# Kernel optimization log

Measured on AMD Instinct MI355X. Metric: run time of the kernel, lower is better.

Reference implementation:

```python
import jax, jax.numpy as jnp
import numpy as np

EMBED_DIM = 512
NUM_HEADS = 8
B, L_Q, L_K = 2, 2048, 2048


def setup_inputs() -> dict:
    key = jax.random.key(0)
    ks = jax.random.split(key, 8)
    s = 0.02  # weight init scale
    return {
        "query": jax.random.normal(ks[0], (B, L_Q, EMBED_DIM), jnp.float32),
        "key":   jax.random.normal(ks[1], (B, L_K, EMBED_DIM), jnp.float32),
        "value": jax.random.normal(ks[2], (B, L_K, EMBED_DIM), jnp.float32),
        "wq": jax.random.normal(ks[3], (EMBED_DIM, EMBED_DIM), jnp.float32) * s,
        "wk": jax.random.normal(ks[4], (EMBED_DIM, EMBED_DIM), jnp.float32) * s,
        "wv": jax.random.normal(ks[5], (EMBED_DIM, EMBED_DIM), jnp.float32) * s,
        "bq": jnp.zeros((EMBED_DIM,), jnp.float32),
        "bk": jnp.zeros((EMBED_DIM,), jnp.float32),
        "bv": jnp.zeros((EMBED_DIM,), jnp.float32),
        "wo": jax.random.normal(ks[6], (EMBED_DIM, EMBED_DIM), jnp.float32) * s,
        "bo": jnp.zeros((EMBED_DIM,), jnp.float32),
    }


def _prob_sparse_mask(query, key, num_heads):
    # Faithful to _prob_QK: max-mean sparsity score, top-k query selection,
    # gather of reduced queries, reduced QK matmul (vectorized, no python loops).
    Bq, Lq, D = query.shape
    Lk = key.shape[1]
    dh = D // num_heads
    n_top = int(np.log(Lk))  # int(np.ceil/np.log) as in source forward: int(np.log(L_K))
    Q = query.reshape(Bq, Lq, num_heads, dh)
    K = key.reshape(Bq, Lk, num_heads, dh)
    Qh = jnp.transpose(Q, (0, 2, 1, 3))                      # [B,H,Lq,dh]
    # NOTE: source does K.transpose(1,2).reshape(B,H,D,L_K) -- a reshape, not a
    # transpose of the last two dims. We replicate that exactly.
    Kr = jnp.transpose(K, (0, 2, 1, 3)).reshape(Bq, num_heads, dh, Lk)  # [B,H,dh,Lk]
    QK = jnp.einsum('bhqd,bhdk->bhqk', Qh, Kr)               # [B,H,Lq,Lk]
    M = QK.max(-1) - QK.sum(-1) / Lk                         # max-mean score [B,H,Lq]
    _, M_top = jax.lax.top_k(M, n_top)                       # [B,H,n_top]
    Q_red = jnp.take_along_axis(Qh, M_top[..., None], axis=2)  # [B,H,n_top,dh]
    QK_red = jnp.einsum('bhtd,bhdk->bhtk', Q_red, Kr)        # [B,H,n_top,Lk]
    # Scatter reduced rows back into a full additive attn mask (zeros elsewhere).
    mask = jnp.zeros((Bq, num_heads, Lq, Lk), QK.dtype)
    bi = jnp.arange(Bq)[:, None, None]
    hi = jnp.arange(num_heads)[None, :, None]
    return mask.at[bi, hi, M_top].set(QK_red)


def reference(query, key, value, wq, wk, wv, bq, bk, bv, wo, bo):
    Bq, Lq, D = query.shape
    Lk = key.shape[1]
    H = NUM_HEADS
    dh = D // H
    mask = _prob_sparse_mask(query, key, H)                  # [B,H,Lq,Lk]
    q = (query @ wq.T + bq).reshape(Bq, Lq, H, dh).transpose(0, 2, 1, 3)
    k = (key @ wk.T + bk).reshape(Bq, Lk, H, dh).transpose(0, 2, 1, 3)
    v = (value @ wv.T + bv).reshape(Bq, Lk, H, dh).transpose(0, 2, 1, 3)
    scores = jnp.einsum('bhqd,bhkd->bhqk', q, k) * (dh ** -0.5) + mask
    attn = jax.nn.softmax(scores, axis=-1)                   # dropout inactive (eval)
    out = jnp.einsum('bhqk,bhkd->bhqd', attn, v)
    out = out.transpose(0, 2, 1, 3).reshape(Bq, Lq, D)
    return out @ wo.T + bo
```

## Files before the change

kernel.cpp:

```cpp
#include <hip/hip_runtime.h>

#define DEV static __device__ __forceinline__

typedef short s16;
typedef __attribute__((ext_vector_type(4))) short short4_t;
typedef __attribute__((ext_vector_type(8))) short short8;
typedef __attribute__((ext_vector_type(4))) float f32x4;

#define NB 2
#define NH 8
#define SL 2048
#define DM 512
#define DH 64
#define NTOP 7
#define LOG2E 1.4426950408889634f
#define NROWS (NB*NH*SL)
#define FSPLIT 2
#define SSPLIT 2

DEV short f2bf(float x){
  union { float f; unsigned u; } v; v.f = x;
  unsigned r = v.u + 0x7fffu + ((v.u >> 16) & 1u);
  return (short)(r >> 16);
}
DEV float bf2f(short b){
  union { float f; unsigned u; } v; v.u = ((unsigned)(unsigned short)b) << 16;
  return v.f;
}
DEV f32x4 mfma16(short8 a, short8 b, f32x4 c){
  return __builtin_amdgcn_mfma_f32_16x16x32_bf16(a, b, c, 0, 0, 0);
}
DEV unsigned cvtpk(float lo, float hi){
  unsigned r;
  asm("v_cvt_pk_bf16_f32 %0, %1, %2" : "=v"(r) : "v"(lo), "v"(hi));
  return r;
}
DEV void gl2lds16(const s16* g, s16* l){
  __builtin_amdgcn_global_load_lds(
      (const __attribute__((address_space(1))) unsigned*)g,
      (__attribute__((address_space(3))) unsigned*)l, 16, 0, 0);
}

__global__ void prep_kernel(const float* __restrict__ query, const float* __restrict__ key,
    const float* __restrict__ value,
    const float* __restrict__ wq, const float* __restrict__ wk,
    const float* __restrict__ wv, const float* __restrict__ wo,
    s16* __restrict__ q_hi, s16* __restrict__ q_lo, s16* __restrict__ xk, s16* __restrict__ xv,
    s16* __restrict__ khi, s16* __restrict__ klo,
    s16* __restrict__ wqb, s16* __restrict__ wkb, s16* __restrict__ wvb, s16* __restrict__ wob){
  const int nbb = (NB*SL*DM)/256;
  const int wbb = (DM*DM)/256;
  __shared__ s16 thi[64][66];
  __shared__ s16 tlo[64][66];
  int bid = blockIdx.x;
  int t = threadIdx.x;
  if (bid < nbb){
    int i = bid*256 + t;
    float v = query[i];
    short h = f2bf(v);
    q_hi[i] = h;
    q_lo[i] = f2bf(v - bf2f(h));
    return;
  }
  bid -= nbb;
  if (bid < nbb){ int i = bid*256 + t; xk[i] = f2bf(key[i]); return; }
  bid -= nbb;
  if (bid < nbb){ int i = bid*256 + t; xv[i] = f2bf(value[i]); return; }
  bid -= nbb;
  if (bid < 512){
    int k6 = bid & 31, h = (bid >> 5) & 7, b = bid >> 8;
    int kl = t & 63, dq = t >> 6;
    #pragma unroll
    for (int dd = 0; dd < 16; ++dd){
      int d = dd*4 + dq;
      float v = key[((size_t)b*SL + d*32 + k6)*DM + h*DH + kl];
      short hh = f2bf(v);
      thi[d][kl] = hh;
      tlo[d][kl] = f2bf(v - bf2f(hh));
    }
    __syncthreads();
    int d2 = t & 63, kq = t >> 6;
    size_t obase = (((size_t)(b*NH + h))*SL + (size_t)k6*64)*DH;
    #pragma unroll
    for (int kk = 0; kk < 16; ++kk){
      int kl2 = kk*4 + kq;
      khi[obase + (size_t)kl2*DH + d2] = thi[d2][kl2];
      klo[obase + (size_t)kl2*DH + d2] = tlo[d2][kl2];
    }
    return;
  }
  bid -= 512;
  if (bid < wbb){ int i = bid*256 + t; wqb[i] = f2bf(wq[i]); return; }
  bid -= wbb;
  if (bid < wbb){ int i = bid*256 + t; wkb[i] = f2bf(wk[i]); return; }
  bid -= wbb;
  if (bid < wbb){ int i = bid*256 + t; wvb[i] = f2bf(wv[i]); return; }
  bid -= wbb;
  if (bid < wbb){ int i = bid*256 + t; wob[i] = f2bf(wo[i]); return; }
}

__global__ __launch_bounds__(256) void vpt_kernel(const s16* __restrict__ Vp, s16* __restrict__ VpT){
  __shared__ s16 tl[64][66];
  int bid = blockIdx.x;
  int k6 = bid & 31, h = (bid >> 5) & 7, b = bid >> 8;
  int t = threadIdx.x;
  int d = t & 63, kq = t >> 6;
  #pragma unroll
  for (int kk = 0; kk < 16; ++kk){
    int kl = kk*4 + kq;
    tl[kl][d] = Vp[((size_t)b*SL + k6*64 + kl)*DM + h*DH + d];
  }
  __syncthreads();
  int kl2 = t & 63, dq = t >> 6;
  size_t obase = ((size_t)(b*NH + h))*DH*SL + (size_t)k6*64;
  #pragma unroll
  for (int dd = 0; dd < 16; ++dd){
    int d2 = dd*4 + dq;
    VpT[obase + (size_t)d2*SL + kl2] = tl[kl2][d2];
  }
}

template<int OUTF32>
DEV void gemm_body(const s16* __restrict__ A, const s16* __restrict__ Bw,
        const float* __restrict__ bias, void* __restrict__ Cout, int bid, int tid, float scale){
  __shared__ __align__(16) s16 Abuf[2][128*64];
  __shared__ __align__(16) s16 Bbuf[2][64*64];
  int nt = bid >> 3, ot = bid & 7;
  int w = tid >> 6, l = tid & 63;
  int lr = l & 15, lg = l >> 4;
  int n0 = nt*128, o0 = ot*64;
  auto stage = [&](int cur, int kg){
    #pragma unroll
    for (int i = 0; i < 4; ++i){
      int r = w*32 + i*8 + (l>>3);
      int cs = (l&7) ^ (r&7);
      gl2lds16(A + (size_t)(n0 + r)*DM + kg + cs*8, &Abuf[cur][(w*32 + i*8)*64]);
    }
    #pragma unroll
    for (int i = 0; i < 2; ++i){
      int r = w*16 + i*8 + (l>>3);
      int cs = (l&7) ^ (r&7);
      gl2lds16(Bw + (size_t)(o0 + r)*DM + kg + cs*8, &Bbuf[cur][(w*16 + i*8)*64]);
    }
  };
  f32x4 acc[2][4] = {};
  stage(0, 0);
  __syncthreads();
  const int NIT = DM/64;
  for (int it = 0; it < NIT; ++it){
    int cur = it & 1;
    if (it + 1 < NIT) stage(cur^1, (it+1)*64);
    #pragma unroll
    for (int kc = 0; kc < 2; ++kc){
      short8 a0 = *(const short8*)&Abuf[cur][(w*32 +      lr)*64 + ((kc*4+lg) ^ (lr&7))*8];
      short8 a1 = *(const short8*)&Abuf[cur][(w*32 + 16 + lr)*64 + ((kc*4+lg) ^ (lr&7))*8];
      #pragma unroll
      for (int c = 0; c < 4; ++c){
        short8 bf = *(const short8*)&Bbuf[cur][(c*16 + lr)*64 + ((kc*4+lg) ^ (lr&7))*8];
        acc[0][c] = mfma16(a0, bf, acc[0][c]);
        acc[1][c] = mfma16(a1, bf, acc[1][c]);
      }
    }
    __syncthreads();
  }
  #pragma unroll
  for (int sub = 0; sub < 2; ++sub)
    #pragma unroll
    for (int c = 0; c < 4; ++c){
      int col = o0 + c*16 + lr;
      float bb = bias[col];
      #pragma unroll
      for (int j = 0; j < 4; ++j){
        int row = n0 + w*32 + sub*16 + lg*4 + j;
        float v = (acc[sub][c][j] + bb)*scale;
        if (OUTF32) ((float*)Cout)[(size_t)row*DM + col] = v;
        else        ((s16*) Cout)[(size_t)row*DM + col] = f2bf(v);
      }
    }
}

__global__ __launch_bounds__(256) void gemm_proj(const s16* __restrict__ Aq, const s16* __restrict__ Ak,
        const s16* __restrict__ Av, const s16* __restrict__ Wq, const s16* __restrict__ Wk,
        const s16* __restrict__ Wv, const float* __restrict__ bq, const float* __restrict__ bk,
        const float* __restrict__ bv, s16* __restrict__ Oq, s16* __restrict__ Ok, s16* __restrict__ Ov){
  int which = blockIdx.x >> 8;
  const s16* A  = which == 0 ? Aq : which == 1 ? Ak : Av;
  const s16* Bw = which == 0 ? Wq : which == 1 ? Wk : Wv;
  const float* bias = which == 0 ? bq : which == 1 ? bk : bv;
  s16* C = which == 0 ? Oq : which == 1 ? Ok : Ov;
  float scale = which == 0 ? 0.125f*LOG2E : 1.0f;
  gemm_body<0>(A, Bw, bias, C, blockIdx.x & 255, threadIdx.x, scale);
}

__global__ __launch_bounds__(256) void gemm_out(const s16* __restrict__ A, const s16* __restrict__ Bw,
        const float* __restrict__ bias, float* __restrict__ Cout){
  gemm_body<1>(A, Bw, bias, Cout, blockIdx.x, threadIdx.x, 1.0f);
}

__global__ __launch_bounds__(256) void stats_kernel(const s16* __restrict__ qhi, const s16* __restrict__ qlo,
        const s16* __restrict__ khi, const s16* __restrict__ klo,
        float* __restrict__ Mmx, float* __restrict__ Msm){
  __shared__ __align__(16) s16 Hbuf[2][64*64];
  __shared__ __align__(16) s16 Lbuf[2][64*64];
  int bid = blockIdx.x;
  int s = bid & 1, qt = (bid >> 1) & 31, h = (bid >> 6) & 7, b = bid >> 9;
  int tid = threadIdx.x;
  int w = tid >> 6, l = tid & 63;
  int lr = l & 15, lg = l >> 4;
  int dx = lr & 7;
  int q0 = qt*64 + w*16;
  const s16* qp  = qhi + ((size_t)b*SL + q0 + lr)*DM + h*DH + lg*8;
  const s16* qlp = qlo + ((size_t)b*SL + q0 + lr)*DM + h*DH + lg*8;
  short8 qh0 = *(const short8*)qp;
  short8 qh1 = *(const short8*)(qp + 32);
  short8 ql0 = *(const short8*)qlp;
  short8 ql1 = *(const short8*)(qlp + 32);
  const s16* kb  = khi + ((size_t)b*NH + h)*SL*DH;
  const s16* klb = klo + ((size_t)b*NH + h)*SL*DH;
  auto stage = [&](int cur, int kg){
    #pragma unroll
    for (int i = 0; i < 2; ++i){
      int r = w*16 + i*8 + (l>>3);
      int cs = (l&7) ^ (r&7);
      gl2lds16(kb  + (size_t)(kg + r)*DH + cs*8, &Hbuf[cur][(w*16 + i*8)*64]);
    }
    #pragma unroll
    for (int i = 0; i < 2; ++i){
      int r = w*16 + i*8 + (l>>3);
      int cs = (l&7) ^ (r&7);
      gl2lds16(klb + (size_t)(kg + r)*DH + cs*8, &Lbuf[cur][(w*16 + i*8)*64]);
    }
  };
  float mx = -1e30f, sm = 0.f;
  int kbeg = s*(SL/SSPLIT);
  const int NIT = (SL/SSPLIT)/64;
  stage(0, kbeg);
  __syncthreads();
  for (int it = 0; it < NIT; ++it){
    int cur = it & 1;
    if (it + 1 < NIT) stage(cur^1, kbeg + (it+1)*64);
    #pragma unroll
    for (int t = 0; t < 4; ++t){
      int rb = (t*16 + lr)*64;
      short8 kh0 = *(const short8*)&Hbuf[cur][rb + ((  lg) ^ dx)*8];
      short8 kh1 = *(const short8*)&Hbuf[cur][rb + ((4+lg) ^ dx)*8];
      short8 kl0 = *(const short8*)&Lbuf[cur][rb + ((  lg) ^ dx)*8];
      short8 kl1 = *(const short8*)&Lbuf[cur][rb + ((4+lg) ^ dx)*8];
      f32x4 sacc = {};
      sacc = mfma16(kh0, qh0, sacc);
      sacc = mfma16(kh1, qh1, sacc);
      sacc = mfma16(kl0, qh0, sacc);
      sacc = mfma16(kl1, qh1, sacc);
      sacc = mfma16(kh0, ql0, sacc);
      sacc = mfma16(kh1, ql1, sacc);
      #pragma unroll
      for (int j = 0; j < 4; ++j){ mx = fmaxf(mx, sacc[j]); sm += sacc[j]; }
    }
    __syncthreads();
  }
  mx = fmaxf(mx, __shfl_xor(mx, 16));
  mx = fmaxf(mx, __shfl_xor(mx, 32));
  sm += __shfl_xor(sm, 16);
  sm += __shfl_xor(sm, 32);
  if (lg == 0){
    size_t row = ((size_t)b*NH + h)*SL + q0 + lr;
    Mmx[(size_t)s*NROWS + row] = mx;
    Msm[(size_t)s*NROWS + row] = sm;
  }
}

__global__ __launch_bounds__(64) void topk_kernel(const float* __restrict__ Mmx,
        const float* __restrict__ Msm, int* __restrict__ topidx, int* __restrict__ rowsel){
  int bh = blockIdx.x;
  int l = threadIdx.x;
  __shared__ float smv[SL];
  size_t base = (size_t)bh*SL;
  for (int i = l; i < SL; i += 64){
    float mx = Mmx[base + i];
    float sm = Msm[base + i];
    #pragma unroll
    for (int s = 1; s < SSPLIT; ++s){
      mx = fmaxf(mx, Mmx[(size_t)s*NROWS + base + i]);
      sm += Msm[(size_t)s*NROWS + base + i];
    }
    smv[i] = mx - sm*(1.0f/SL);
    rowsel[base + i] = -1;
  }
  __syncthreads();
  for (int t = 0; t < NTOP; ++t){
    float bvv = -1e38f; int bi = SL;
    for (int i = l; i < SL; i += 64){
      float v = smv[i];
      if (v > bvv){ bvv = v; bi = i; }
    }
    for (int off = 32; off >= 1; off >>= 1){
      float ov = __shfl_xor(bvv, off);
      int oi = __shfl_xor(bi, off);
      if (ov > bvv || (ov == bvv && oi < bi)){ bvv = ov; bi = oi; }
    }
    if (l == 0){
      topidx[bh*8 + t] = bi;
      rowsel[base + bi] = t;
    }
    smv[bi] = -1e38f;
    __syncthreads();
  }
}

__global__ __launch_bounds__(256) void maskrow_kernel(const float* __restrict__ query,
        const float* __restrict__ key, const int* __restrict__ topidx, float* __restrict__ maskrows){
  __shared__ float tile[64][65];
  __shared__ float qs[NTOP][64];
  int bid = blockIdx.x;
  int k6 = bid & 31, h = (bid >> 5) & 7, b = bid >> 8;
  int bh = b*NH + h;
  int t = threadIdx.x;
  int kl = t & 63, w = t >> 6;
  for (int i = t; i < NTOP*64; i += 256){
    int tt = i >> 6, d = i & 63;
    qs[tt][d] = query[((size_t)b*SL + topidx[bh*8 + tt])*DM + h*DH + d];
  }
  #pragma unroll
  for (int dd = 0; dd < 16; ++dd){
    int d = dd*4 + w;
    tile[d][kl] = key[((size_t)b*SL + d*32 + k6)*DM + h*DH + kl];
  }
  __syncthreads();
  for (int tt = w; tt < NTOP; tt += 4){
    float acc = 0.f;
    #pragma unroll
    for (int d = 0; d < 64; ++d)
      acc = fmaf(qs[tt][d], tile[d][kl], acc);
    maskrows[((size_t)bh*NTOP + tt)*SL + k6*64 + kl] = acc*LOG2E;
  }
}

__global__ __launch_bounds__(256) void flash_kernel(const s16* __restrict__ Qp, const s16* __restrict__ Kp,
        const s16* __restrict__ VpT, const float* __restrict__ maskrows, const int* __restrict__ rowsel,
        float* __restrict__ Opart, float* __restrict__ lpart){
  __shared__ __align__(16) s16 Kbuf[2][64*64];
  __shared__ __align__(16) s16 Vbuf[2][64*64];
  int bid = blockIdx.x;
  int s = bid & 1, qt = (bid >> 1) & 31, h = (bid >> 6) & 7, b = bid >> 9;
  int tid = threadIdx.x;
  int w = tid >> 6, l = tid & 63;
  int lr = l & 15, lg = l >> 4;
  int dx = lr & 7;
  int q0 = qt*64 + w*16;
  int bh = b*NH + h;
  const s16* qp = Qp + ((size_t)b*SL + q0 + lr)*DM + h*DH + lg*8;
  short8 bq0 = *(const short8*)qp;
  short8 bq1 = *(const short8*)(qp + 32);
  int sel = rowsel[(size_t)bh*SL + q0 + lr];
  const float* mrow = maskrows + ((size_t)bh*NTOP + (sel >= 0 ? sel : 0))*SL;
  const s16* kpb = Kp + (size_t)b*SL*DM + h*DH;
  const s16* vtb = VpT + (size_t)bh*DH*SL;
  auto stage = [&](int cur, int kg){
    #pragma unroll
    for (int i = 0; i < 2; ++i){
      int r = w*16 + i*8 + (l>>3);
      int cs = (l&7) ^ (r&7);
      gl2lds16(kpb + (size_t)(kg + r)*DM + cs*8, &Kbuf[cur][(w*16 + i*8)*64]);
    }
    #pragma unroll
    for (int i = 0; i < 2; ++i){
      int d = w*16 + i*8 + (l>>3);
      int cs = (l&7) ^ (d&7);
      gl2lds16(vtb + (size_t)d*SL + kg + cs*8, &Vbuf[cur][(w*16 + i*8)*64]);
    }
  };
  f32x4 acc[4] = {};
  float lsum = 0.f;
  int kbeg = s*(SL/FSPLIT);
  const int NIT = (SL/FSPLIT)/64;
  stage(0, kbeg);
  __syncthreads();
  for (int it = 0; it < NIT; ++it){
    int cur = it & 1;
    if (it + 1 < NIT) stage(cur^1, kbeg + (it+1)*64);
    int k0 = kbeg + it*64;
    float pv[4][4];
    #pragma unroll
    for (int t = 0; t < 4; ++t){
      int rb = (t*16 + lr)*64;
      short8 ka0 = *(const short8*)&Kbuf[cur][rb + ((  lg) ^ dx)*8];
      short8 ka1 = *(const short8*)&Kbuf[cur][rb + ((4+lg) ^ dx)*8];
      f32x4 sc = {};
      sc = mfma16(ka0, bq0, sc);
      sc = mfma16(ka1, bq1, sc);
      #pragma unroll
      for (int j = 0; j < 4; ++j) pv[t][j] = sc[j];
    }
    if (sel >= 0){
      #pragma unroll
      for (int t = 0; t < 4; ++t)
        #pragma unroll
        for (int j = 0; j < 4; ++j)
          pv[t][j] += mrow[k0 + t*16 + lg*4 + j];
    }
    #pragma unroll
    for (int t = 0; t < 4; ++t)
      #pragma unroll
      for (int j = 0; j < 4; ++j){
        float pp = exp2f(pv[t][j]);
        pv[t][j] = pp;
        lsum += pp;
      }
    short8 paf[2];
    #pragma unroll
    for (int kt = 0; kt < 2; ++kt){
      union { unsigned u[4]; short8 s8; } uu;
      uu.u[0] = cvtpk(pv[2*kt][0],   pv[2*kt][1]);
      uu.u[1] = cvtpk(pv[2*kt][2],   pv[2*kt][3]);
      uu.u[2] = cvtpk(pv[2*kt+1][0], pv[2*kt+1][1]);
      uu.u[3] = cvtpk(pv[2*kt+1][2], pv[2*kt+1][3]);
      paf[kt] = uu.s8;
    }
    #pragma unroll
    for (int c = 0; c < 4; ++c){
      const s16* vb = &Vbuf[cur][(c*16 + lr)*64];
      #pragma unroll
      for (int kt = 0; kt < 2; ++kt){
        short4_t lo = *(const short4_t*)&vb[((8*kt   + lg) ^ (dx<<1))*4];
        short4_t hi = *(const short4_t*)&vb[((8*kt+4 + lg) ^ (dx<<1))*4];
        short8 vf = __builtin_shufflevector(lo, hi, 0, 1, 2, 3, 4, 5, 6, 7);
        acc[c] = mfma16(vf, paf[kt], acc[c]);
      }
    }
    __syncthreads();
  }
  lsum += __shfl_xor(lsum, 16);
  lsum += __shfl_xor(lsum, 32);
  size_t row = (size_t)bh*SL + q0 + lr;
  float* Op = Opart + ((size_t)s*NROWS + row)*DH;
  #pragma unroll
  for (int c = 0; c < 4; ++c)
    *(f32x4*)(Op + c*16 + lg*4) = acc[c];
  if (lg == 0)
    lpart[(size_t)s*NROWS + row] = lsum;
}

__global__ __launch_bounds__(256) void flash_combine(const float* __restrict__ Opart,
        const float* __restrict__ lpart, s16* __restrict__ outh){
  int row = blockIdx.x*4 + (threadIdx.x >> 6);
  int d = threadIdx.x & 63;
  float L = lpart[row] + lpart[NROWS + row];
  float o = (Opart[(size_t)row*DH + d] + Opart[((size_t)NROWS + row)*DH + d]) / L;
  int b = row >> 14, h = (row >> 11) & 7, q = row & (SL - 1);
  outh[((size_t)b*SL + q)*DM + h*DH + d] = f2bf(o);
}

extern "C" void kernel_launch(void* const* d_in, const int* in_sizes, int n_in,
                              void* d_out, int out_size, void* d_ws, size_t ws_size,
                              hipStream_t stream){
  (void)in_sizes; (void)n_in; (void)out_size;
  const float* query = (const float*)d_in[0];
  const float* key   = (const float*)d_in[1];
  const float* value = (const float*)d_in[2];
  const float* wq    = (const float*)d_in[3];
  const float* wk    = (const float*)d_in[4];
  const float* wv    = (const float*)d_in[5];
  const float* bq    = (const float*)d_in[6];
  const float* bk    = (const float*)d_in[7];
  const float* bv    = (const float*)d_in[8];
  const float* wo    = (const float*)d_in[9];
  const float* bo    = (const float*)d_in[10];

  const size_t NE = (size_t)NB*SL*DM;
  const size_t WE = (size_t)DM*DM;

  char* p = (char*)d_ws;
  size_t off = 0;
  auto alloc = [&](size_t n)->char*{ char* r = p + off; off += (n + 255) & ~(size_t)255; return r; };
  s16* wob = (s16*)alloc(WE*2);
  s16* Qp  = (s16*)alloc(NE*2);
  s16* Kp  = (s16*)alloc(NE*2);
  s16* VpT = (s16*)alloc(NE*2);
  float* maskrows = (float*)alloc((size_t)NB*NH*NTOP*SL*4);
  int* topidx   = (int*)alloc((size_t)NB*NH*8*4);
  int* rowsel   = (int*)alloc((size_t)NROWS*4);
  float* Mmx    = (float*)alloc((size_t)SSPLIT*NROWS*4);
  float* Msm    = (float*)alloc((size_t)SSPLIT*NROWS*4);
  float* lpart  = (float*)alloc((size_t)FSPLIT*NROWS*4);
  s16* outh = (s16*)alloc(NE*2);
  size_t offA = off;
  s16* q_hi = (s16*)alloc(NE*2);
  s16* q_lo = (s16*)alloc(NE*2);
  s16* xk   = (s16*)alloc(NE*2);
  s16* xv   = (s16*)alloc(NE*2);
  s16* khatT_hi = (s16*)alloc(NE*2);
  s16* khatT_lo = (s16*)alloc(NE*2);
  s16* wqb = (s16*)alloc(WE*2);
  s16* wkb = (s16*)alloc(WE*2);
  s16* wvb = (s16*)alloc(WE*2);
  s16* Vp  = (s16*)alloc(NE*2);
  float* Opart = (float*)(p + offA);
  size_t needOpart = offA + (size_t)FSPLIT*NROWS*DH*4;
  if (off > ws_size || needOpart > ws_size) return;

  const int nbb = (int)(NE/256);
  const int wbb = (int)(WE/256);
  prep_kernel<<<3*nbb + 512 + 4*wbb, 256, 0, stream>>>(query, key, value, wq, wk, wv, wo,
      q_hi, q_lo, xk, xv, khatT_hi, khatT_lo, wqb, wkb, wvb, wob);

  gemm_proj<<<3*256, 256, 0, stream>>>(q_hi, xk, xv, wqb, wkb, wvb, bq, bk, bv, Qp, Kp, Vp);
  vpt_kernel<<<512, 256, 0, stream>>>(Vp, VpT);

  stats_kernel<<<NB*NH*(SL/64)*SSPLIT, 256, 0, stream>>>(q_hi, q_lo, khatT_hi, khatT_lo, Mmx, Msm);
  topk_kernel<<<NB*NH, 64, 0, stream>>>(Mmx, Msm, topidx, rowsel);
  maskrow_kernel<<<512, 256, 0, stream>>>(query, key, topidx, maskrows);

  flash_kernel<<<NB*NH*(SL/64)*FSPLIT, 256, 0, stream>>>(Qp, Kp, VpT, maskrows, rowsel,
      Opart, lpart);
  flash_combine<<<NROWS/4, 256, 0, stream>>>(Opart, lpart, outh);
  gemm_out<<<256, 256, 0, stream>>>(outh, wob, bo, (float*)d_out);
}
```

Before: 165.0 us.

## Use 128-row query tiles with 8 waves in stats and flash kernels

Measured after the change: 139.9 us. -15.2%, faster.

```diff
diff --git a/kernel.cpp b/kernel.cpp
--- a/kernel.cpp
+++ b/kernel.cpp
@@ -1,4 +1,5 @@
 #include <hip/hip_runtime.h>
+#include <type_traits>
 
 #define DEV static __device__ __forceinline__
 
@@ -197,18 +198,18 @@
   gemm_body<1>(A, Bw, bias, Cout, blockIdx.x, threadIdx.x, 1.0f);
 }
 
-__global__ __launch_bounds__(256) void stats_kernel(const s16* __restrict__ qhi, const s16* __restrict__ qlo,
+__global__ __launch_bounds__(512) void stats_kernel(const s16* __restrict__ qhi, const s16* __restrict__ qlo,
         const s16* __restrict__ khi, const s16* __restrict__ klo,
         float* __restrict__ Mmx, float* __restrict__ Msm){
   __shared__ __align__(16) s16 Hbuf[2][64*64];
   __shared__ __align__(16) s16 Lbuf[2][64*64];
   int bid = blockIdx.x;
-  int s = bid & 1, qt = (bid >> 1) & 31, h = (bid >> 6) & 7, b = bid >> 9;
+  int s = bid & 1, qt = (bid >> 1) & 15, h = (bid >> 5) & 7, b = bid >> 8;
   int tid = threadIdx.x;
   int w = tid >> 6, l = tid & 63;
   int lr = l & 15, lg = l >> 4;
   int dx = lr & 7;
-  int q0 = qt*64 + w*16;
+  int q0 = qt*128 + w*16;
   const s16* qp  = qhi + ((size_t)b*SL + q0 + lr)*DM + h*DH + lg*8;
   const s16* qlp = qlo + ((size_t)b*SL + q0 + lr)*DM + h*DH + lg*8;
   short8 qh0 = *(const short8*)qp;
@@ -217,35 +218,25 @@
   short8 ql1 = *(const short8*)(qlp + 32);
   const s16* kb  = khi + ((size_t)b*NH + h)*SL*DH;
   const s16* klb = klo + ((size_t)b*NH + h)*SL*DH;
+  const s16* hR0 = &Hbuf[0][lr*64 + ((lg      ^ dx)*8)];
+  const s16* hR1 = &Hbuf[0][lr*64 + (((4+lg) ^ dx)*8)];
+  const s16* lR0 = &Lbuf[0][lr*64 + ((lg      ^ dx)*8)];
+  const s16* lR1 = &Lbuf[0][lr*64 + (((4+lg) ^ dx)*8)];
+  int rS = tid >> 3;
+  int csK = (tid & 7) ^ (rS & 7);
   auto stage = [&](int cur, int kg){
-    #pragma unroll
-    for (int i = 0; i < 2; ++i){
-      int r = w*16 + i*8 + (l>>3);
-      int cs = (l&7) ^ (r&7);
-      gl2lds16(kb  + (size_t)(kg + r)*DH + cs*8, &Hbuf[cur][(w*16 + i*8)*64]);
-    }
-    #pragma unroll
-    for (int i = 0; i < 2; ++i){
-      int r = w*16 + i*8 + (l>>3);
-      int cs = (l&7) ^ (r&7);
-      gl2lds16(klb + (size_t)(kg + r)*DH + cs*8, &Lbuf[cur][(w*16 + i*8)*64]);
-    }
+    gl2lds16(kb  + (size_t)(kg + rS)*DH + csK*8, &Hbuf[cur][w*512]);
+    gl2lds16(klb + (size_t)(kg + rS)*DH + csK*8, &Lbuf[cur][w*512]);
   };
   float mx = -1e30f, sm = 0.f;
-  int kbeg = s*(SL/SSPLIT);
-  const int NIT = (SL/SSPLIT)/64;
-  stage(0, kbeg);
-  __syncthreads();
-  for (int it = 0; it < NIT; ++it){
-    int cur = it & 1;
-    if (it + 1 < NIT) stage(cur^1, kbeg + (it+1)*64);
+  auto body = [&](auto CURC){
+    constexpr int CUR = decltype(CURC)::value;
     #pragma unroll
     for (int t = 0; t < 4; ++t){
-      int rb = (t*16 + lr)*64;
-      short8 kh0 = *(const short8*)&Hbuf[cur][rb + ((  lg) ^ dx)*8];
-      short8 kh1 = *(const short8*)&Hbuf[cur][rb + ((4+lg) ^ dx)*8];
-      short8 kl0 = *(const short8*)&Lbuf[cur][rb + ((  lg) ^ dx)*8];
-      short8 kl1 = *(const short8*)&Lbuf[cur][rb + ((4+lg) ^ dx)*8];
+      short8 kh0 = *(const short8*)(hR0 + CUR*4096 + t*1024);
+      short8 kh1 = *(const short8*)(hR1 + CUR*4096 + t*1024);
+      short8 kl0 = *(const short8*)(lR0 + CUR*4096 + t*1024);
+      short8 kl1 = *(const short8*)(lR1 + CUR*4096 + t*1024);
       f32x4 sacc = {};
       sacc = mfma16(kh0, qh0, sacc);
       sacc = mfma16(kh1, qh1, sacc);
@@ -256,6 +247,17 @@
       #pragma unroll
       for (int j = 0; j < 4; ++j){ mx = fmaxf(mx, sacc[j]); sm += sacc[j]; }
     }
+  };
+  int kbeg = s*(SL/SSPLIT);
+  stage(0, kbeg);
+  __syncthreads();
+  #pragma unroll 1
+  for (int i2 = 0; i2 < 8; ++i2){
+    stage(1, kbeg + (2*i2+1)*64);
+    body(std::integral_constant<int,0>{});
+    __syncthreads();
+    if (i2 < 7) stage(0, kbeg + (2*i2+2)*64);
+    body(std::integral_constant<int,1>{});
     __syncthreads();
   }
   mx = fmaxf(mx, __shfl_xor(mx, 16));
@@ -269,13 +271,16 @@
   }
 }
 
-__global__ __launch_bounds__(64) void topk_kernel(const float* __restrict__ Mmx,
+__global__ __launch_bounds__(256) void topk_kernel(const float* __restrict__ Mmx,
         const float* __restrict__ Msm, int* __restrict__ topidx, int* __restrict__ rowsel){
   int bh = blockIdx.x;
-  int l = threadIdx.x;
+  int t = threadIdx.x;
+  int w = t >> 6, l = t & 63;
   __shared__ float smv[SL];
+  __shared__ float rv[4];
+  __shared__ int   ri[4];
   size_t base = (size_t)bh*SL;
-  for (int i = l; i < SL; i += 64){
+  for (int i = t; i < SL; i += 256){
     float mx = Mmx[base + i];
     float sm = Msm[base + i];
     #pragma unroll
@@ -287,22 +292,29 @@
     rowsel[base + i] = -1;
   }
   __syncthreads();
-  for (int t = 0; t < NTOP; ++t){
+  for (int tt = 0; tt < NTOP; ++tt){
     float bvv = -1e38f; int bi = SL;
-    for (int i = l; i < SL; i += 64){
+    for (int i = t; i < SL; i += 256){
       float v = smv[i];
       if (v > bvv){ bvv = v; bi = i; }
     }
+    #pragma unroll
     for (int off = 32; off >= 1; off >>= 1){
       float ov = __shfl_xor(bvv, off);
       int oi = __shfl_xor(bi, off);
       if (ov > bvv || (ov == bvv && oi < bi)){ bvv = ov; bi = oi; }
     }
-    if (l == 0){
-      topidx[bh*8 + t] = bi;
-      rowsel[base + bi] = t;
-    }
-    smv[bi] = -1e38f;
+    if (l == 0){ rv[w] = bvv; ri[w] = bi; }
+    __syncthreads();
+    if (t == 0){
+      float bv2 = rv[0]; int bi2 = ri[0];
+      #pragma unroll
+      for (int ww = 1; ww < 4; ++ww)
+        if (rv[ww] > bv2 || (rv[ww] == bv2 && ri[ww] < bi2)){ bv2 = rv[ww]; bi2 = ri[ww]; }
+      topidx[bh*8 + tt] = bi2;
+      rowsel[base + bi2] = tt;
+      smv[bi2] = -1e38f;
+    }
     __syncthreads();
   }
 }
@@ -335,18 +347,18 @@
   }
 }
 
-__global__ __launch_bounds__(256) void flash_kernel(const s16* __restrict__ Qp, const s16* __restrict__ Kp,
+__global__ __launch_bounds__(512) void flash_kernel(const s16* __restrict__ Qp, const s16* __restrict__ Kp,
         const s16* __restrict__ VpT, const float* __restrict__ maskrows, const int* __restrict__ rowsel,
         float* __restrict__ Opart, float* __restrict__ lpart){
   __shared__ __align__(16) s16 Kbuf[2][64*64];
   __shared__ __align__(16) s16 Vbuf[2][64*64];
   int bid = blockIdx.x;
-  int s = bid & 1, qt = (bid >> 1) & 31, h = (bid >> 6) & 7, b = bid >> 9;
+  int s = bid & 1, qt = (bid >> 1) & 15, h = (bid >> 5) & 7, b = bid >> 8;
   int tid = threadIdx.x;
   int w = tid >> 6, l = tid & 63;
   int lr = l & 15, lg = l >> 4;
   int dx = lr & 7;
-  int q0 = qt*64 + w*16;
+  int q0 = qt*128 + w*16;
   int bh = b*NH + h;
   const s16* qp = Qp + ((size_t)b*SL + q0 + lr)*DM + h*DH + lg*8;
   short8 bq0 = *(const short8*)qp;
@@ -355,36 +367,28 @@
   const float* mrow = maskrows + ((size_t)bh*NTOP + (sel >= 0 ? sel : 0))*SL;
   const s16* kpb = Kp + (size_t)b*SL*DM + h*DH;
   const s16* vtb = VpT + (size_t)bh*DH*SL;
+  const s16* kR0 = &Kbuf[0][lr*64 + ((lg      ^ dx)*8)];
+  const s16* kR1 = &Kbuf[0][lr*64 + (((4+lg) ^ dx)*8)];
+  const s16* vb0 = &Vbuf[0][lr*64];
+  const int gL0 = ((0  + lg) ^ (dx<<1))*4;
+  const int gH0 = ((4  + lg) ^ (dx<<1))*4;
+  const int gL1 = ((8  + lg) ^ (dx<<1))*4;
+  const int gH1 = ((12 + lg) ^ (dx<<1))*4;
+  int rS = tid >> 3;
+  int csK = (tid & 7) ^ (rS & 7);
   auto stage = [&](int cur, int kg){
-    #pragma unroll
-    for (int i = 0; i < 2; ++i){
-      int r = w*16 + i*8 + (l>>3);
-      int cs = (l&7) ^ (r&7);
-      gl2lds16(kpb + (size_t)(kg + r)*DM + cs*8, &Kbuf[cur][(w*16 + i*8)*64]);
-    }
-    #pragma unroll
-    for (int i = 0; i < 2; ++i){
-      int d = w*16 + i*8 + (l>>3);
-      int cs = (l&7) ^ (d&7);
-      gl2lds16(vtb + (size_t)d*SL + kg + cs*8, &Vbuf[cur][(w*16 + i*8)*64]);
-    }
+    gl2lds16(kpb + (size_t)(kg + rS)*DM + csK*8, &Kbuf[cur][w*512]);
+    gl2lds16(vtb + (size_t)rS*SL + kg + csK*8, &Vbuf[cur][w*512]);
   };
   f32x4 acc[4] = {};
   float lsum = 0.f;
-  int kbeg = s*(SL/FSPLIT);
-  const int NIT = (SL/FSPLIT)/64;
-  stage(0, kbeg);
-  __syncthreads();
-  for (int it = 0; it < NIT; ++it){
-    int cur = it & 1;
-    if (it + 1 < NIT) stage(cur^1, kbeg + (it+1)*64);
-    int k0 = kbeg + it*64;
+  auto body = [&](auto CURC, int k0){
+    constexpr int CUR = decltype(CURC)::value;
     float pv[4][4];
     #pragma unroll
     for (int t = 0; t < 4; ++t){
-      int rb = (t*16 + lr)*64;
-      short8 ka0 = *(const short8*)&Kbuf[cur][rb + ((  lg) ^ dx)*8];
-      short8 ka1 = *(const short8*)&Kbuf[cur][rb + ((4+lg) ^ dx)*8];
+      short8 ka0 = *(const short8*)(kR0 + CUR*4096 + t*1024);
+      short8 ka1 = *(const short8*)(kR1 + CUR*4096 + t*1024);
       f32x4 sc = {};
       sc = mfma16(ka0, bq0, sc);
       sc = mfma16(ka1, bq1, sc);
@@ -418,15 +422,24 @@
     }
     #pragma unroll
     for (int c = 0; c < 4; ++c){
-      const s16* vb = &Vbuf[cur][(c*16 + lr)*64];
-      #pragma unroll
-      for (int kt = 0; kt < 2; ++kt){
-        short4_t lo = *(const short4_t*)&vb[((8*kt   + lg) ^ (dx<<1))*4];
-        short4_t hi = *(const short4_t*)&vb[((8*kt+4 + lg) ^ (dx<<1))*4];
-        short8 vf = __builtin_shufflevector(lo, hi, 0, 1, 2, 3, 4, 5, 6, 7);
-        acc[c] = mfma16(vf, paf[kt], acc[c]);
-      }
-    }
+      short4_t lo0 = *(const short4_t*)(vb0 + CUR*4096 + c*1024 + gL0);
+      short4_t hi0 = *(const short4_t*)(vb0 + CUR*4096 + c*1024 + gH0);
+      acc[c] = mfma16(__builtin_shufflevector(lo0, hi0, 0,1,2,3,4,5,6,7), paf[0], acc[c]);
+      short4_t lo1 = *(const short4_t*)(vb0 + CUR*4096 + c*1024 + gL1);
+      short4_t hi1 = *(const short4_t*)(vb0 + CUR*4096 + c*1024 + gH1);
+      acc[c] = mfma16(__builtin_shufflevector(lo1, hi1, 0,1,2,3,4,5,6,7), paf[1], acc[c]);
+    }
+  };
+  int kbeg = s*(SL/FSPLIT);
+  stage(0, kbeg);
+  __syncthreads();
+  #pragma unroll 1
+  for (int i2 = 0; i2 < 8; ++i2){
+    stage(1, kbeg + (2*i2+1)*64);
+    body(std::integral_constant<int,0>{}, kbeg + 2*i2*64);
+    __syncthreads();
+    if (i2 < 7) stage(0, kbeg + (2*i2+2)*64);
+    body(std::integral_constant<int,1>{}, kbeg + (2*i2+1)*64);
     __syncthreads();
   }
   lsum += __shfl_xor(lsum, 16);
@@ -506,11 +519,11 @@
   gemm_proj<<<3*256, 256, 0, stream>>>(q_hi, xk, xv, wqb, wkb, wvb, bq, bk, bv, Qp, Kp, Vp);
   vpt_kernel<<<512, 256, 0, stream>>>(Vp, VpT);
 
-  stats_kernel<<<NB*NH*(SL/64)*SSPLIT, 256, 0, stream>>>(q_hi, q_lo, khatT_hi, khatT_lo, Mmx, Msm);
-  topk_kernel<<<NB*NH, 64, 0, stream>>>(Mmx, Msm, topidx, rowsel);
+  stats_kernel<<<NB*NH*(SL/128)*SSPLIT, 512, 0, stream>>>(q_hi, q_lo, khatT_hi, khatT_lo, Mmx, Msm);
+  topk_kernel<<<NB*NH, 256, 0, stream>>>(Mmx, Msm, topidx, rowsel);
   maskrow_kernel<<<512, 256, 0, stream>>>(query, key, topidx, maskrows);
 
-  flash_kernel<<<NB*NH*(SL/64)*FSPLIT, 256, 0, stream>>>(Qp, Kp, VpT, maskrows, rowsel,
+  flash_kernel<<<NB*NH*(SL/128)*FSPLIT, 512, 0, stream>>>(Qp, Kp, VpT, maskrows, rowsel,
       Opart, lpart);
   flash_combine<<<NROWS/4, 256, 0, stream>>>(Opart, lpart, outh);
   gemm_out<<<256, 256, 0, stream>>>(outh, wob, bo, (float*)d_out);
```
